# Optimization experiments

Measured on AMD Instinct MI355X. Metric: run time of the kernel, lower is better.

## Reference

```python
import jax, jax.numpy as jnp
import numpy as np

BS, LX, LY, D, H, DK = 2, 2048, 2048, 1024, 16, 64


def setup_inputs() -> dict:
    key = jax.random.key(0)
    ks = jax.random.split(key, 12)
    s = 1.0 / np.sqrt(D)
    return {
        "x": jax.random.normal(ks[0], (BS, LX, D), jnp.float32),
        "y": jax.random.normal(ks[1], (BS, LY, D), jnp.float32),
        "mask": jnp.zeros((BS, 1, LX, LY), jnp.float32),
        "Wq": jax.random.normal(ks[2], (D, H * DK), jnp.float32) * s,
        "bq": jnp.zeros((H * DK,), jnp.float32),
        "Wk": jax.random.normal(ks[3], (D, H * DK), jnp.float32) * s,
        "bk": jnp.zeros((H * DK,), jnp.float32),
        "Wv": jax.random.normal(ks[4], (D, H * DK), jnp.float32) * s,
        "bv": jnp.zeros((H * DK,), jnp.float32),
        "Wo": jax.random.normal(ks[5], (H * DK, D), jnp.float32) * s,
        "bo": jnp.zeros((D,), jnp.float32),
    }


def reference(x, y, mask, Wq, bq, Wk, bk, Wv, bv, Wo, bo):
    bs, lx, _ = x.shape
    ly = y.shape[1]
    norm = DK ** 0.5
    # projections -> (bs, len, H, DK)
    q = (x @ Wq + bq).reshape(bs, lx, H, DK)
    k = (y @ Wk + bk).reshape(bs, ly, H, DK)
    v = (y @ Wv + bv).reshape(bs, ly, H, DK)
    # scores: (bs, H, lx, ly)
    scores = jnp.einsum('bxhd,byhd->bhxy', q, k) / norm + mask
    attn = jax.nn.softmax(scores, axis=-1)
    # output: (bs, lx, H, DK) -> (bs, lx, H*DK)
    out = jnp.einsum('bhxy,byhd->bxhd', attn, v).reshape(bs, lx, H * DK)
    return out @ Wo + bo
```

## Files before the change

### kernel.cpp

```cpp
#include <hip/hip_runtime.h>
#include <hip/hip_bf16.h>


typedef __bf16 bf16;
typedef __bf16 bf16x4 __attribute__((ext_vector_type(4)));
typedef __bf16 bf16x8 __attribute__((ext_vector_type(8)));
typedef float floatx4 __attribute__((ext_vector_type(4)));

#define MFMA16(a, b, c) __builtin_amdgcn_mfma_f32_16x16x32_bf16(a, b, c, 0, 0, 0)

constexpr int BS = 2, LX = 2048, LY = 2048, D = 1024, H = 16, DK = 64;
constexpr int HD = H * DK;
constexpr float LOG2E = 1.4426950408889634f;

__device__ __forceinline__ void cp16(const bf16* g, bf16* l) {
  __builtin_amdgcn_global_load_lds(
      (const __attribute__((address_space(1))) unsigned int*)g,
      (__attribute__((address_space(3))) unsigned int*)l, 16, 0, 0);
}

__global__ __launch_bounds__(256) void prep(const float* __restrict__ W0, bf16* __restrict__ T0,
                                            const float* __restrict__ W1, bf16* __restrict__ T1,
                                            const float* __restrict__ W2, bf16* __restrict__ T2,
                                            const float* __restrict__ W3, bf16* __restrict__ T3,
                                            const float* __restrict__ x, bf16* __restrict__ xb,
                                            const float* __restrict__ y, bf16* __restrict__ yb,
                                            const float* __restrict__ mask, int* __restrict__ flags) {
  const int id = blockIdx.x;
  const int t = threadIdx.x;
  if (id < 1024) {
    __shared__ bf16 tile[64][72];
    const float* W;
    bf16* T;
    switch (id >> 8) {
      case 0: W = W0; T = T0; break;
      case 1: W = W1; T = T1; break;
      case 2: W = W2; T = T2; break;
      default: W = W3; T = T3; break;
    }
    const int kt = id & 15, nt = (id >> 4) & 15;
    const int r = t >> 2, c4 = (t & 3) * 16;
    const float* src = W + (size_t)(kt * 64 + r) * 1024 + nt * 64 + c4;
#pragma unroll
    for (int i = 0; i < 16; i++) tile[r][c4 + i] = (bf16)src[i];
    __syncthreads();
    bf16 vals[16];
#pragma unroll
    for (int i = 0; i < 16; i++) vals[i] = tile[c4 + i][r];
    bf16* dst = T + (size_t)(nt * 64 + r) * 1024 + kt * 64 + c4;
#pragma unroll
    for (int i = 0; i < 16; i++) dst[i] = vals[i];
  } else if (id < 5120) {
    const int id2 = id - 1024;
    const float* src = (id2 >= 2048) ? y : x;
    bf16* dst = (id2 >= 2048) ? yb : xb;
    const size_t i = ((size_t)(id2 & 2047) * 256 + t) * 8;
    float4 a = *(const float4*)(src + i);
    float4 c = *(const float4*)(src + i + 4);
    bf16 tmp[8] = {(bf16)a.x, (bf16)a.y, (bf16)a.z, (bf16)a.w,
                   (bf16)c.x, (bf16)c.y, (bf16)c.z, (bf16)c.w};
    *(bf16x8*)(dst + i) = *(const bf16x8*)tmp;
  } else {
    const int id3 = id - 5120;
    const int region = id3 >> 5, sub = id3 & 31;
    const float4* p = (const float4*)mask + (size_t)region * 65536 + sub * 2048;
    bool nz = false;
#pragma unroll
    for (int it = 0; it < 8; it++) {
      float4 v = p[it * 256 + t];
      nz |= (v.x != 0.f) | (v.y != 0.f) | (v.z != 0.f) | (v.w != 0.f);
    }
    if (nz) atomicOr(&flags[region], 1);
  }
}

__global__ __launch_bounds__(256) void qkv_gemm(const bf16* __restrict__ xb, const bf16* __restrict__ yb,
                                                const bf16* __restrict__ Wtq, const bf16* __restrict__ Wtk,
                                                const bf16* __restrict__ Wtv,
                                                const float* __restrict__ bq, const float* __restrict__ bk,
                                                const float* __restrict__ bv,
                                                bf16* __restrict__ Qb, bf16* __restrict__ Kb,
                                                bf16* __restrict__ Vt) {
  constexpr int K = 1024, N = 1024;
  __shared__ __align__(16) bf16 smem[128 * 136];
  bf16* As = smem;
  bf16* Bs = smem + 128 * 64;
  bf16* Ct = smem;

  const int z = blockIdx.z;
  const bf16* A = (z == 0) ? xb : yb;
  const bf16* Bt = (z == 0) ? Wtq : (z == 1) ? Wtk : Wtv;
  const float* bias = (z == 0) ? bq : (z == 1) ? bk : bv;

  const int t = threadIdx.x;
  const int w = t >> 6, lane = t & 63, quad = lane >> 4, l15 = lane & 15;
  const int wr = (w & 1) * 64, wc = (w >> 1) * 64;
  const int mbase = blockIdx.y * 128, nbase = blockIdx.x * 128;
  const int srow = lane >> 3, schunk = (lane & 7) ^ srow;
  const int sx = quad ^ (l15 & 7);

  floatx4 acc[4][4] = {};

  for (int k0 = 0; k0 < K; k0 += 64) {
    __syncthreads();
#pragma unroll
    for (int j = 0; j < 4; j++) {
      const int r0 = w * 32 + j * 8;
      cp16(A + (size_t)(mbase + r0 + srow) * K + k0 + schunk * 8, As + r0 * 64);
      cp16(Bt + (size_t)(nbase + r0 + srow) * K + k0 + schunk * 8, Bs + r0 * 64);
    }
    __syncthreads();
    bf16x8 af[4][2], bfr[4][2];
#pragma unroll
    for (int i = 0; i < 4; i++) {
      const int ra = wr + i * 16 + l15;
      af[i][0] = *(const bf16x8*)&As[ra * 64 + sx * 8];
      af[i][1] = *(const bf16x8*)&As[ra * 64 + (sx ^ 4) * 8];
      const int rb = wc + i * 16 + l15;
      bfr[i][0] = *(const bf16x8*)&Bs[rb * 64 + sx * 8];
      bfr[i][1] = *(const bf16x8*)&Bs[rb * 64 + (sx ^ 4) * 8];
    }
#pragma unroll
    for (int i = 0; i < 4; i++)
#pragma unroll
      for (int jn = 0; jn < 4; jn++) {
        acc[i][jn] = MFMA16(af[i][0], bfr[jn][0], acc[i][jn]);
        acc[i][jn] = MFMA16(af[i][1], bfr[jn][1], acc[i][jn]);
      }
  }

  if (z <= 1) {
    bf16* outp = (z == 0) ? Qb : Kb;
    const float sc = (z == 0) ? 0.125f * LOG2E : 1.0f;
#pragma unroll
    for (int jn = 0; jn < 4; jn++) {
      const int n = nbase + wc + jn * 16 + l15;
      const float bv2 = bias[n];
#pragma unroll
      for (int i = 0; i < 4; i++)
#pragma unroll
        for (int r = 0; r < 4; r++) {
          const int m = mbase + wr + i * 16 + quad * 4 + r;
          outp[(size_t)m * N + n] = (bf16)((acc[i][jn][r] + bv2) * sc);
        }
    }
  } else {
    __syncthreads();
#pragma unroll
    for (int jn = 0; jn < 4; jn++) {
      const int nl = wc + jn * 16 + l15;
      const float bv2 = bias[nbase + nl];
#pragma unroll
      for (int i = 0; i < 4; i++)
#pragma unroll
        for (int r = 0; r < 4; r++) {
          const int ml = wr + i * 16 + quad * 4 + r;
          Ct[nl * 136 + ml] = (bf16)(acc[i][jn][r] + bv2);
        }
    }
    __syncthreads();
    const int n = t >> 1, mh = (t & 1) * 64;
    const int gn = nbase + n;
    const int hh = gn >> 6, dk = gn & 63;
    const int bb = mbase >> 11, y0 = (mbase & 2047) + mh;
    bf16* dst = Vt + ((size_t)(bb * H + hh) * DK + dk) * LY + y0;
    const bf16* srcr = &Ct[n * 136 + mh];
#pragma unroll
    for (int u = 0; u < 8; u++) *(bf16x8*)(dst + u * 8) = *(const bf16x8*)(srcr + u * 8);
  }
}

__global__ __launch_bounds__(256) void out_gemm(const bf16* __restrict__ A, const bf16* __restrict__ Bt,
                                                const float* __restrict__ bias, float* __restrict__ outp) {
  constexpr int K = 1024, N = 1024;
  __shared__ __align__(16) bf16 As[128 * 64];
  __shared__ __align__(16) bf16 Bs[64 * 64];
  const int t = threadIdx.x;
  const int w = t >> 6, lane = t & 63, quad = lane >> 4, l15 = lane & 15;
  const int mbase = blockIdx.y * 128, nbase = blockIdx.x * 64;
  const int srow = lane >> 3, schunk = (lane & 7) ^ srow;
  const int sx = quad ^ (l15 & 7);

  floatx4 acc[2][4] = {};
  for (int k0 = 0; k0 < K; k0 += 64) {
    __syncthreads();
#pragma unroll
    for (int j = 0; j < 4; j++) {
      const int r0 = w * 32 + j * 8;
      cp16(A + (size_t)(mbase + r0 + srow) * K + k0 + schunk * 8, As + r0 * 64);
    }
#pragma unroll
    for (int j = 0; j < 2; j++) {
      const int r0 = w * 16 + j * 8;
      cp16(Bt + (size_t)(nbase + r0 + srow) * K + k0 + schunk * 8, Bs + r0 * 64);
    }
    __syncthreads();
    bf16x8 af[2][2], bfr[4][2];
#pragma unroll
    for (int i = 0; i < 2; i++) {
      const int ra = w * 32 + i * 16 + l15;
      af[i][0] = *(const bf16x8*)&As[ra * 64 + sx * 8];
      af[i][1] = *(const bf16x8*)&As[ra * 64 + (sx ^ 4) * 8];
    }
#pragma unroll
    for (int jn = 0; jn < 4; jn++) {
      const int rb = jn * 16 + l15;
      bfr[jn][0] = *(const bf16x8*)&Bs[rb * 64 + sx * 8];
      bfr[jn][1] = *(const bf16x8*)&Bs[rb * 64 + (sx ^ 4) * 8];
    }
#pragma unroll
    for (int i = 0; i < 2; i++)
#pragma unroll
      for (int jn = 0; jn < 4; jn++) {
        acc[i][jn] = MFMA16(af[i][0], bfr[jn][0], acc[i][jn]);
        acc[i][jn] = MFMA16(af[i][1], bfr[jn][1], acc[i][jn]);
      }
  }
#pragma unroll
  for (int jn = 0; jn < 4; jn++) {
    const int n = nbase + jn * 16 + l15;
    const float bv2 = bias[n];
#pragma unroll
    for (int i = 0; i < 2; i++)
#pragma unroll
      for (int r = 0; r < 4; r++) {
        const int m = mbase + w * 32 + i * 16 + quad * 4 + r;
        outp[(size_t)m * N + n] = acc[i][jn][r] + bv2;
      }
  }
}

__global__ __launch_bounds__(256, 2) void attn5(const bf16* __restrict__ Q, const bf16* __restrict__ Kb,
                                                const bf16* __restrict__ Vt, const float* __restrict__ mask,
                                                const int* __restrict__ flags, bf16* __restrict__ Hout) {
  __shared__ __align__(16) bf16 Ks[2][64 * 64];
  __shared__ __align__(16) bf16 Vs[2][64 * 64];
  __shared__ __align__(16) bf16 Plds[4][32 * 72];
  const int t = threadIdx.x;
  const int w = t >> 6, lane = t & 63, quad = lane >> 4, l15 = lane & 15;
  const int xt = blockIdx.x, h = blockIdx.y, b = blockIdx.z;
  const int qbase = xt * 128 + w * 32;
  const int srow = lane >> 3, schunk = (lane & 7) ^ srow;
  const int sx = quad ^ (l15 & 7);

  bf16x8 qf[2][2];
#pragma unroll
  for (int rt = 0; rt < 2; rt++) {
    const bf16* qrow = Q + (size_t)(b * LX + qbase + rt * 16 + l15) * HD + h * DK;
    qf[rt][0] = *(const bf16x8*)(qrow + quad * 8);
    qf[rt][1] = *(const bf16x8*)(qrow + 32 + quad * 8);
  }
  const int mflag = flags[b * 16 + xt];

  bf16 onearr[8];
#pragma unroll
  for (int i = 0; i < 8; i++) onearr[i] = (bf16)((l15 == 0) ? 1.0f : 0.0f);
  const bf16x8 onesf = *(const bf16x8*)onearr;

  floatx4 o[2][4] = {};
  floatx4 ol[2] = {};

  const bf16* Kbase = Kb + (size_t)b * LY * HD + h * DK;
  const bf16* Vbase = Vt + (size_t)(b * H + h) * DK * LY;
  const float* mbase2 = mask + (size_t)(b * LX + qbase + l15) * LY;

#define STAGE(yt, bufi)                                                               \
  {                                                                                   \
    _Pragma("unroll") for (int j = 0; j < 2; j++) {                                   \
      const int r0 = w * 16 + j * 8;                                                  \
      cp16(Kbase + (size_t)((yt) + r0 + srow) * HD + schunk * 8, &Ks[bufi][r0 * 64]); \
      cp16(Vbase + (size_t)(r0 + srow) * LY + (yt) + schunk * 8, &Vs[bufi][r0 * 64]); \
    }                                                                                 \
  }

#define TILE(yt, BUF)                                                                  \
  {                                                                                    \
    const bf16* KsB = Ks[BUF];                                                         \
    const bf16* VsB = Vs[BUF];                                                         \
    bf16x8 kf[4][2];                                                                   \
    _Pragma("unroll") for (int nt = 0; nt < 4; nt++) {                                 \
      const int ry = nt * 16 + l15;                                                    \
      kf[nt][0] = *(const bf16x8*)&KsB[ry * 64 + sx * 8];                              \
      kf[nt][1] = *(const bf16x8*)&KsB[ry * 64 + (sx ^ 4) * 8];                        \
    }                                                                                  \
    floatx4 s[2][4] = {};                                                              \
    _Pragma("unroll") for (int nt = 0; nt < 4; nt++)                                   \
        _Pragma("unroll") for (int rt = 0; rt < 2; rt++) {                             \
      s[rt][nt] = MFMA16(kf[nt][0], qf[rt][0], s[rt][nt]);                             \
      s[rt][nt] = MFMA16(kf[nt][1], qf[rt][1], s[rt][nt]);                             \
    }                                                                                  \
    if (mflag) {                                                                       \
      _Pragma("unroll") for (int rt = 0; rt < 2; rt++)                                 \
          _Pragma("unroll") for (int nt = 0; nt < 4; nt++) {                           \
        const float* mp = mbase2 + (size_t)rt * 16 * LY + (yt) + nt * 16 + quad * 4;   \
        float4 mv = *(const float4*)mp;                                                \
        s[rt][nt][0] = fminf(s[rt][nt][0] + LOG2E * mv.x, 30.f);                       \
        s[rt][nt][1] = fminf(s[rt][nt][1] + LOG2E * mv.y, 30.f);                       \
        s[rt][nt][2] = fminf(s[rt][nt][2] + LOG2E * mv.z, 30.f);                       \
        s[rt][nt][3] = fminf(s[rt][nt][3] + LOG2E * mv.w, 30.f);                       \
      }                                                                                \
    }                                                                                  \
    _Pragma("unroll") for (int rt = 0; rt < 2; rt++)                                   \
        _Pragma("unroll") for (int nt = 0; nt < 4; nt++) {                             \
      bf16x4 pk;                                                                       \
      _Pragma("unroll") for (int r = 0; r < 4; r++) pk[r] = (bf16)exp2f(s[rt][nt][r]); \
      *(bf16x4*)&Plds[w][(rt * 16 + l15) * 72 + nt * 16 + quad * 4] = pk;              \
    }                                                                                  \
    bf16x8 pf[2][2];                                                                   \
    _Pragma("unroll") for (int rt = 0; rt < 2; rt++) {                                 \
      const bf16* prow = &Plds[w][(rt * 16 + l15) * 72];                               \
      pf[rt][0] = *(const bf16x8*)(prow + quad * 8);                                   \
      pf[rt][1] = *(const bf16x8*)(prow + 32 + quad * 8);                              \
    }                                                                                  \
    _Pragma("unroll") for (int u = 0; u < 4; u++) {                                    \
      const int rd = u * 16 + l15;                                                     \
      bf16x8 v0 = *(const bf16x8*)&VsB[rd * 64 + sx * 8];                              \
      bf16x8 v1 = *(const bf16x8*)&VsB[rd * 64 + (sx ^ 4) * 8];                        \
      _Pragma("unroll") for (int rt = 0; rt < 2; rt++) {                               \
        o[rt][u] = MFMA16(pf[rt][0], v0, o[rt][u]);                                    \
        o[rt][u] = MFMA16(pf[rt][1], v1, o[rt][u]);                                    \
      }                                                                                \
    }                                                                                  \
    _Pragma("unroll") for (int rt = 0; rt < 2; rt++) {                                 \
      ol[rt] = MFMA16(pf[rt][0], onesf, ol[rt]);                                       \
      ol[rt] = MFMA16(pf[rt][1], onesf, ol[rt]);                                       \
    }                                                                                  \
  }

  STAGE(0, 0);
  for (int yt = 0; yt < LY; yt += 128) {
    __syncthreads();
    STAGE(yt + 64, 1);
    TILE(yt, 0);
    __syncthreads();
    if (yt + 128 < LY) STAGE(yt + 128, 0);
    TILE(yt + 64, 1);
  }

#pragma unroll
  for (int rt = 0; rt < 2; rt++)
#pragma unroll
    for (int r = 0; r < 4; r++) {
      const float lsum = __shfl(ol[rt][r], lane & 48, 64);
      const float rl = 1.0f / lsum;
      const int m = b * LX + qbase + rt * 16 + quad * 4 + r;
#pragma unroll
      for (int u = 0; u < 4; u++)
        Hout[(size_t)m * HD + h * DK + u * 16 + l15] = (bf16)(o[rt][u][r] * rl);
    }
#undef STAGE
#undef TILE
}

extern "C" void kernel_launch(void* const* d_in, const int* in_sizes, int n_in,
                              void* d_out, int out_size, void* d_ws, size_t ws_size,
                              hipStream_t stream) {
  const float* x = (const float*)d_in[0];
  const float* y = (const float*)d_in[1];
  const float* mask = (const float*)d_in[2];
  const float* Wq = (const float*)d_in[3];
  const float* bq = (const float*)d_in[4];
  const float* Wk = (const float*)d_in[5];
  const float* bk = (const float*)d_in[6];
  const float* Wv = (const float*)d_in[7];
  const float* bv = (const float*)d_in[8];
  const float* Wo = (const float*)d_in[9];
  const float* bo = (const float*)d_in[10];

  char* ws = (char*)d_ws;
  size_t off = 0;
  bf16* Qb = (bf16*)(ws + off); off += (size_t)BS * LX * HD * 2;
  bf16* Kb = (bf16*)(ws + off); off += (size_t)BS * LY * HD * 2;
  bf16* Vt = (bf16*)(ws + off); off += (size_t)BS * LY * HD * 2;
  bf16* Hb = (bf16*)(ws + off); off += (size_t)BS * LX * HD * 2;
  bf16* xbf = (bf16*)(ws + off); off += (size_t)BS * LX * D * 2;
  bf16* ybf = (bf16*)(ws + off); off += (size_t)BS * LY * D * 2;
  bf16* Wtq = (bf16*)(ws + off); off += (size_t)D * HD * 2;
  bf16* Wtk = (bf16*)(ws + off); off += (size_t)D * HD * 2;
  bf16* Wtv = (bf16*)(ws + off); off += (size_t)D * HD * 2;
  bf16* Wto = (bf16*)(ws + off); off += (size_t)HD * D * 2;
  int* flags = (int*)(ws + off); off += 32 * sizeof(int);

  dim3 blk(256);
  hipMemsetAsync(flags, 0, 32 * sizeof(int), stream);
  prep<<<dim3(6144), blk, 0, stream>>>(Wq, Wtq, Wk, Wtk, Wv, Wtv, Wo, Wto, x, xbf, y, ybf, mask, flags);
  qkv_gemm<<<dim3(8, 32, 3), blk, 0, stream>>>(xbf, ybf, Wtq, Wtk, Wtv, bq, bk, bv, Qb, Kb, Vt);
  attn5<<<dim3(16, 16, 2), blk, 0, stream>>>(Qb, Kb, Vt, mask, flags, Hb);
  out_gemm<<<dim3(16, 32), blk, 0, stream>>>(Hb, Wto, bo, (float*)d_out);
}
```

Measured before the change: 249.5 us.

## Split attention over key dimension into two halves and merge partial outputs

Attention blocks now each handle half of the key/value sequence, which doubles the grid from 512 to 1024 blocks for better CU occupancy. Unnormalized partial outputs and row sums go to workspace that reuses the dead xbf/ybf region, and a new hmerge kernel sums both halves and normalizes. The per-tile schedule is also changed: V is single-buffered, P is staged per row tile, and launch_bounds no longer requests 2 blocks per CU. The cost is an extra launch and an extra pass over the partial outputs in memory. Because there is no running max, the halves can be summed directly, and the same approach was already used before.

Measured after the change: 265.9 us. 1.07x slower.

```diff
diff --git a/kernel.cpp b/kernel.cpp
--- a/kernel.cpp
+++ b/kernel.cpp
@@ -230,16 +230,19 @@
   }
 }
 
-__global__ __launch_bounds__(256, 2) void attn5(const bf16* __restrict__ Q, const bf16* __restrict__ Kb,
-                                                const bf16* __restrict__ Vt, const float* __restrict__ mask,
-                                                const int* __restrict__ flags, bf16* __restrict__ Hout) {
+__global__ __launch_bounds__(256) void attn6(const bf16* __restrict__ Q, const bf16* __restrict__ Kb,
+                                             const bf16* __restrict__ Vt, const float* __restrict__ mask,
+                                             const int* __restrict__ flags, bf16* __restrict__ OP,
+                                             float* __restrict__ LP) {
   __shared__ __align__(16) bf16 Ks[2][64 * 64];
-  __shared__ __align__(16) bf16 Vs[2][64 * 64];
-  __shared__ __align__(16) bf16 Plds[4][32 * 72];
+  __shared__ __align__(16) bf16 Vs[64 * 64];
+  __shared__ __align__(16) bf16 Plds[4][16 * 72];
   const int t = threadIdx.x;
   const int w = t >> 6, lane = t & 63, quad = lane >> 4, l15 = lane & 15;
-  const int xt = blockIdx.x, h = blockIdx.y, b = blockIdx.z;
+  const int xt = blockIdx.x, h = blockIdx.y;
+  const int b = blockIdx.z >> 1, split = blockIdx.z & 1;
   const int qbase = xt * 128 + w * 32;
+  const int y0 = split * 1024;
   const int srow = lane >> 3, schunk = (lane & 7) ^ srow;
   const int sx = quad ^ (l15 & 7);
 
@@ -260,96 +263,128 @@
   floatx4 o[2][4] = {};
   floatx4 ol[2] = {};
 
-  const bf16* Kbase = Kb + (size_t)b * LY * HD + h * DK;
-  const bf16* Vbase = Vt + (size_t)(b * H + h) * DK * LY;
-  const float* mbase2 = mask + (size_t)(b * LX + qbase + l15) * LY;
-
-#define STAGE(yt, bufi)                                                               \
-  {                                                                                   \
-    _Pragma("unroll") for (int j = 0; j < 2; j++) {                                   \
-      const int r0 = w * 16 + j * 8;                                                  \
-      cp16(Kbase + (size_t)((yt) + r0 + srow) * HD + schunk * 8, &Ks[bufi][r0 * 64]); \
-      cp16(Vbase + (size_t)(r0 + srow) * LY + (yt) + schunk * 8, &Vs[bufi][r0 * 64]); \
-    }                                                                                 \
-  }
-
-#define TILE(yt, BUF)                                                                  \
-  {                                                                                    \
-    const bf16* KsB = Ks[BUF];                                                         \
-    const bf16* VsB = Vs[BUF];                                                         \
-    bf16x8 kf[4][2];                                                                   \
-    _Pragma("unroll") for (int nt = 0; nt < 4; nt++) {                                 \
-      const int ry = nt * 16 + l15;                                                    \
-      kf[nt][0] = *(const bf16x8*)&KsB[ry * 64 + sx * 8];                              \
-      kf[nt][1] = *(const bf16x8*)&KsB[ry * 64 + (sx ^ 4) * 8];                        \
-    }                                                                                  \
-    floatx4 s[2][4] = {};                                                              \
-    _Pragma("unroll") for (int nt = 0; nt < 4; nt++)                                   \
-        _Pragma("unroll") for (int rt = 0; rt < 2; rt++) {                             \
-      s[rt][nt] = MFMA16(kf[nt][0], qf[rt][0], s[rt][nt]);                             \
-      s[rt][nt] = MFMA16(kf[nt][1], qf[rt][1], s[rt][nt]);                             \
-    }                                                                                  \
-    if (mflag) {                                                                       \
-      _Pragma("unroll") for (int rt = 0; rt < 2; rt++)                                 \
-          _Pragma("unroll") for (int nt = 0; nt < 4; nt++) {                           \
-        const float* mp = mbase2 + (size_t)rt * 16 * LY + (yt) + nt * 16 + quad * 4;   \
-        float4 mv = *(const float4*)mp;                                                \
-        s[rt][nt][0] = fminf(s[rt][nt][0] + LOG2E * mv.x, 30.f);                       \
-        s[rt][nt][1] = fminf(s[rt][nt][1] + LOG2E * mv.y, 30.f);                       \
-        s[rt][nt][2] = fminf(s[rt][nt][2] + LOG2E * mv.z, 30.f);                       \
-        s[rt][nt][3] = fminf(s[rt][nt][3] + LOG2E * mv.w, 30.f);                       \
-      }                                                                                \
-    }                                                                                  \
-    _Pragma("unroll") for (int rt = 0; rt < 2; rt++)                                   \
-        _Pragma("unroll") for (int nt = 0; nt < 4; nt++) {                             \
-      bf16x4 pk;                                                                       \
-      _Pragma("unroll") for (int r = 0; r < 4; r++) pk[r] = (bf16)exp2f(s[rt][nt][r]); \
-      *(bf16x4*)&Plds[w][(rt * 16 + l15) * 72 + nt * 16 + quad * 4] = pk;              \
-    }                                                                                  \
-    bf16x8 pf[2][2];                                                                   \
-    _Pragma("unroll") for (int rt = 0; rt < 2; rt++) {                                 \
-      const bf16* prow = &Plds[w][(rt * 16 + l15) * 72];                               \
-      pf[rt][0] = *(const bf16x8*)(prow + quad * 8);                                   \
-      pf[rt][1] = *(const bf16x8*)(prow + 32 + quad * 8);                              \
-    }                                                                                  \
-    _Pragma("unroll") for (int u = 0; u < 4; u++) {                                    \
-      const int rd = u * 16 + l15;                                                     \
-      bf16x8 v0 = *(const bf16x8*)&VsB[rd * 64 + sx * 8];                              \
-      bf16x8 v1 = *(const bf16x8*)&VsB[rd * 64 + (sx ^ 4) * 8];                        \
-      _Pragma("unroll") for (int rt = 0; rt < 2; rt++) {                               \
-        o[rt][u] = MFMA16(pf[rt][0], v0, o[rt][u]);                                    \
-        o[rt][u] = MFMA16(pf[rt][1], v1, o[rt][u]);                                    \
-      }                                                                                \
-    }                                                                                  \
-    _Pragma("unroll") for (int rt = 0; rt < 2; rt++) {                                 \
-      ol[rt] = MFMA16(pf[rt][0], onesf, ol[rt]);                                       \
-      ol[rt] = MFMA16(pf[rt][1], onesf, ol[rt]);                                       \
-    }                                                                                  \
-  }
-
-  STAGE(0, 0);
-  for (int yt = 0; yt < LY; yt += 128) {
-    __syncthreads();
-    STAGE(yt + 64, 1);
-    TILE(yt, 0);
-    __syncthreads();
-    if (yt + 128 < LY) STAGE(yt + 128, 0);
-    TILE(yt + 64, 1);
-  }
-
-#pragma unroll
-  for (int rt = 0; rt < 2; rt++)
+  const bf16* Kbase = Kb + (size_t)(b * LY + y0) * HD + h * DK;
+  const bf16* Vbase = Vt + (size_t)(b * H + h) * DK * LY + y0;
+  const float* mbase2 = mask + (size_t)(b * LX + qbase + l15) * LY + y0;
+
+#define STAGE_K(tt, bufi)                                                                    \
+  {                                                                                          \
+    _Pragma("unroll") for (int j = 0; j < 2; j++) {                                          \
+      const int r0 = w * 16 + j * 8;                                                         \
+      cp16(Kbase + (size_t)((tt)*64 + r0 + srow) * HD + schunk * 8, &Ks[bufi][r0 * 64]);     \
+    }                                                                                        \
+  }
+#define STAGE_V(tt)                                                                          \
+  {                                                                                          \
+    _Pragma("unroll") for (int j = 0; j < 2; j++) {                                          \
+      const int r0 = w * 16 + j * 8;                                                         \
+      cp16(Vbase + (size_t)(r0 + srow) * LY + (tt)*64 + schunk * 8, &Vs[r0 * 64]);           \
+    }                                                                                        \
+  }
+
+  STAGE_K(0, 0);
+  STAGE_V(0);
+
+  int buf = 0;
+  for (int tt = 0; tt < 16; tt++) {
+    __syncthreads();
+    if (tt + 1 < 16) STAGE_K(tt + 1, buf ^ 1);
+
+    bf16x8 kf[4][2];
+#pragma unroll
+    for (int nt = 0; nt < 4; nt++) {
+      const int ry = nt * 16 + l15;
+      kf[nt][0] = *(const bf16x8*)&Ks[buf][ry * 64 + sx * 8];
+      kf[nt][1] = *(const bf16x8*)&Ks[buf][ry * 64 + (sx ^ 4) * 8];
+    }
+    floatx4 s[2][4] = {};
+#pragma unroll
+    for (int nt = 0; nt < 4; nt++)
+#pragma unroll
+      for (int rt = 0; rt < 2; rt++) {
+        s[rt][nt] = MFMA16(kf[nt][0], qf[rt][0], s[rt][nt]);
+        s[rt][nt] = MFMA16(kf[nt][1], qf[rt][1], s[rt][nt]);
+      }
+    if (mflag) {
+#pragma unroll
+      for (int rt = 0; rt < 2; rt++)
+#pragma unroll
+        for (int nt = 0; nt < 4; nt++) {
+          const float* mp = mbase2 + (size_t)rt * 16 * LY + tt * 64 + nt * 16 + quad * 4;
+          float4 mv = *(const float4*)mp;
+          s[rt][nt][0] = fminf(s[rt][nt][0] + LOG2E * mv.x, 30.f);
+          s[rt][nt][1] = fminf(s[rt][nt][1] + LOG2E * mv.y, 30.f);
+          s[rt][nt][2] = fminf(s[rt][nt][2] + LOG2E * mv.z, 30.f);
+          s[rt][nt][3] = fminf(s[rt][nt][3] + LOG2E * mv.w, 30.f);
+        }
+    }
+
+    bf16x8 vf[4][2];
+#pragma unroll
+    for (int u = 0; u < 4; u++) {
+      const int rd = u * 16 + l15;
+      vf[u][0] = *(const bf16x8*)&Vs[rd * 64 + sx * 8];
+      vf[u][1] = *(const bf16x8*)&Vs[rd * 64 + (sx ^ 4) * 8];
+    }
+
+#pragma unroll
+    for (int rt = 0; rt < 2; rt++) {
+#pragma unroll
+      for (int nt = 0; nt < 4; nt++) {
+        bf16x4 pk;
+#pragma unroll
+        for (int r = 0; r < 4; r++) pk[r] = (bf16)exp2f(s[rt][nt][r]);
+        *(bf16x4*)&Plds[w][l15 * 72 + nt * 16 + quad * 4] = pk;
+      }
+      const bf16* prow = &Plds[w][l15 * 72];
+      bf16x8 p0 = *(const bf16x8*)(prow + quad * 8);
+      bf16x8 p1 = *(const bf16x8*)(prow + 32 + quad * 8);
+#pragma unroll
+      for (int u = 0; u < 4; u++) {
+        o[rt][u] = MFMA16(p0, vf[u][0], o[rt][u]);
+        o[rt][u] = MFMA16(p1, vf[u][1], o[rt][u]);
+      }
+      ol[rt] = MFMA16(p0, onesf, ol[rt]);
+      ol[rt] = MFMA16(p1, onesf, ol[rt]);
+    }
+
+    __syncthreads();
+    if (tt + 1 < 16) STAGE_V(tt + 1);
+    buf ^= 1;
+  }
+
+  bf16* OPp = OP + (size_t)split * BS * LX * HD;
+  float* LPp = LP + (size_t)split * BS * H * LX;
+#pragma unroll
+  for (int rt = 0; rt < 2; rt++) {
 #pragma unroll
     for (int r = 0; r < 4; r++) {
-      const float lsum = __shfl(ol[rt][r], lane & 48, 64);
-      const float rl = 1.0f / lsum;
       const int m = b * LX + qbase + rt * 16 + quad * 4 + r;
 #pragma unroll
       for (int u = 0; u < 4; u++)
-        Hout[(size_t)m * HD + h * DK + u * 16 + l15] = (bf16)(o[rt][u][r] * rl);
-    }
-#undef STAGE
-#undef TILE
+        OPp[(size_t)m * HD + h * DK + u * 16 + l15] = (bf16)o[rt][u][r];
+    }
+    if (l15 == 0)
+      *(floatx4*)&LPp[(size_t)(b * H + h) * LX + qbase + rt * 16 + quad * 4] = ol[rt];
+  }
+#undef STAGE_K
+#undef STAGE_V
+}
+
+__global__ __launch_bounds__(256) void hmerge(const bf16* __restrict__ OP, const float* __restrict__ LP,
+                                              bf16* __restrict__ Hb) {
+  const size_t i8 = ((size_t)blockIdx.x * 256 + threadIdx.x) * 8;
+  const bf16x8 a = *(const bf16x8*)(OP + i8);
+  const bf16x8 b = *(const bf16x8*)(OP + (size_t)BS * LX * HD + i8);
+  const int bb = (int)(i8 >> 21);
+  const int x = (int)(i8 >> 10) & 2047;
+  const int h = (int)(i8 >> 6) & 15;
+  const size_t li = (size_t)(bb * H + h) * LX + x;
+  const float rl = 1.0f / (LP[li] + LP[(size_t)BS * H * LX + li]);
+  bf16 outv[8];
+#pragma unroll
+  for (int j = 0; j < 8; j++) outv[j] = (bf16)(((float)a[j] + (float)b[j]) * rl);
+  *(bf16x8*)(Hb + i8) = *(const bf16x8*)outv;
 }
 
 extern "C" void kernel_launch(void* const* d_in, const int* in_sizes, int n_in,
@@ -369,22 +404,26 @@
 
   char* ws = (char*)d_ws;
   size_t off = 0;
+  int* flags = (int*)(ws + off); off += 256;
   bf16* Qb = (bf16*)(ws + off); off += (size_t)BS * LX * HD * 2;
   bf16* Kb = (bf16*)(ws + off); off += (size_t)BS * LY * HD * 2;
   bf16* Vt = (bf16*)(ws + off); off += (size_t)BS * LY * HD * 2;
   bf16* Hb = (bf16*)(ws + off); off += (size_t)BS * LX * HD * 2;
+  const size_t region = off;
   bf16* xbf = (bf16*)(ws + off); off += (size_t)BS * LX * D * 2;
   bf16* ybf = (bf16*)(ws + off); off += (size_t)BS * LY * D * 2;
   bf16* Wtq = (bf16*)(ws + off); off += (size_t)D * HD * 2;
   bf16* Wtk = (bf16*)(ws + off); off += (size_t)D * HD * 2;
   bf16* Wtv = (bf16*)(ws + off); off += (size_t)D * HD * 2;
   bf16* Wto = (bf16*)(ws + off); off += (size_t)HD * D * 2;
-  int* flags = (int*)(ws + off); off += 32 * sizeof(int);
+  bf16* OP = (bf16*)(ws + region);
+  float* LP = (float*)(ws + region + (size_t)2 * BS * LX * HD * 2);
 
   dim3 blk(256);
   hipMemsetAsync(flags, 0, 32 * sizeof(int), stream);
   prep<<<dim3(6144), blk, 0, stream>>>(Wq, Wtq, Wk, Wtk, Wv, Wtv, Wo, Wto, x, xbf, y, ybf, mask, flags);
   qkv_gemm<<<dim3(8, 32, 3), blk, 0, stream>>>(xbf, ybf, Wtq, Wtk, Wtv, bq, bk, bv, Qb, Kb, Vt);
-  attn5<<<dim3(16, 16, 2), blk, 0, stream>>>(Qb, Kb, Vt, mask, flags, Hb);
+  attn6<<<dim3(16, 16, 4), blk, 0, stream>>>(Qb, Kb, Vt, mask, flags, OP, LP);
+  hmerge<<<dim3(2048), blk, 0, stream>>>(OP, LP, Hb);
   out_gemm<<<dim3(16, 32), blk, 0, stream>>>(Hb, Wto, bo, (float*)d_out);
 }
```
